# Kernel tuning notes

Hardware: AMD Instinct MI355X
Metric: run time of the kernel (lower is better)

Reference implementation:

```python
import jax, jax.numpy as jnp
import numpy as np

N, E, B_GRAPHS = 50000, 512000, 64
XD, ED, C, H, L = 16, 8, 64, 2, 2
EPS = 1e-5


def setup_inputs() -> dict:
    key = jax.random.key(0)
    ks = jax.random.split(key, 20)
    w = lambda k, shape: jax.random.normal(k, shape, jnp.float32) * 0.1
    return {
        "x": jax.random.normal(ks[0], (N, XD), jnp.float32),
        "edge_attr": jax.random.normal(ks[1], (E, ED), jnp.float32),
        "edge_src": jax.random.randint(ks[2], (E,), 0, N, dtype=jnp.int32),
        "edge_dst": jax.random.randint(ks[3], (E,), 0, N, dtype=jnp.int32),
        "batch": jnp.sort(jax.random.randint(ks[4], (N,), 0, B_GRAPHS, dtype=jnp.int32)),
        "node_W": w(ks[5], (XD, C)), "node_b": jnp.zeros((C,), jnp.float32),
        "edge_W": w(ks[6], (ED, C)), "edge_b": jnp.zeros((C,), jnp.float32),
        "Wq": w(ks[7], (L, C, H * C)), "bq": jnp.zeros((L, H * C), jnp.float32),
        "Wk": w(ks[8], (L, C, H * C)), "bk": jnp.zeros((L, H * C), jnp.float32),
        "Wv": w(ks[9], (L, C, H * C)), "bv": jnp.zeros((L, H * C), jnp.float32),
        "We": w(ks[10], (L, C, H * C)), "be": jnp.zeros((L, H * C), jnp.float32),
        "Wskip": w(ks[11], (L, C, C)), "bskip": jnp.zeros((L, C), jnp.float32),
        "gamma": jnp.ones((L, C), jnp.float32), "beta": jnp.zeros((L, C), jnp.float32),
        "gate_W": w(ks[12], (C, 1)), "gate_b": jnp.zeros((1,), jnp.float32),
        "out_W": w(ks[13], (C, 1)), "out_b": jnp.zeros((1,), jnp.float32),
    }


def reference(x, edge_attr, edge_src, edge_dst, batch,
              node_W, node_b, edge_W, edge_b,
              Wq, bq, Wk, bk, Wv, bv, We, be,
              Wskip, bskip, gamma, beta,
              gate_W, gate_b, out_W, out_b):
    n = x.shape[0]
    h = x @ node_W + node_b                       # node encoder: [N, C]
    e = edge_attr @ edge_W + edge_b               # edge encoder: [E, C]
    scale = 1.0 / jnp.sqrt(jnp.float32(C))
    for i in range(L):
        identity = h
        # TransformerConv (UniMP), concat=False -> mean over heads
        q = (h @ Wq[i] + bq[i]).reshape(n, H, C)
        k = (h @ Wk[i] + bk[i]).reshape(n, H, C)
        v = (h @ Wv[i] + bv[i]).reshape(n, H, C)
        ep = (e @ We[i] + be[i]).reshape(-1, H, C)
        k_e = k[edge_src] + ep                    # [E, H, C]
        v_e = v[edge_src] + ep                    # [E, H, C]
        logits = jnp.einsum('ehc,ehc->eh', q[edge_dst], k_e) * scale
        # segment softmax over incoming edges of each target node
        m = jax.ops.segment_max(logits, edge_dst, num_segments=n)
        a = jnp.exp(logits - m[edge_dst])
        denom = jax.ops.segment_sum(a, edge_dst, num_segments=n)
        alpha = a / denom[edge_dst]               # [E, H]
        agg = jax.ops.segment_sum(alpha[:, :, None] * v_e, edge_dst, num_segments=n)
        out = agg.mean(axis=1) + h @ Wskip[i] + bskip[i]   # root/skip term
        # BatchNorm1d (training mode, biased variance)
        mu = out.mean(axis=0)
        var = out.var(axis=0)
        out = gamma[i] * (out - mu) * jax.lax.rsqrt(var + EPS) + beta[i]
        out = jax.nn.leaky_relu(out, 0.01)
        h = out + identity                        # residual
    # GlobalAttention pooling over graphs
    gate = (h @ gate_W + gate_b)[:, 0]            # [N]
    gm = jax.ops.segment_max(gate, batch, num_segments=B_GRAPHS)
    ge = jnp.exp(gate - gm[batch])
    gd = jax.ops.segment_sum(ge, batch, num_segments=B_GRAPHS)
    wts = ge / gd[batch]
    pooled = jax.ops.segment_sum(wts[:, None] * h, batch, num_segments=B_GRAPHS)
    return jax.nn.sigmoid(pooled @ out_W + out_b)  # [B_GRAPHS, 1]
```

## Files before the change

kernel.cpp:

```cpp
#include <hip/hip_runtime.h>
#include <hip/hip_bf16.h>

typedef unsigned short ushort_t;
typedef __attribute__((ext_vector_type(8))) short short8;
typedef __attribute__((ext_vector_type(4))) float float4v;

__device__ __forceinline__ float bfu_lo(unsigned u) {
    return __uint_as_float(u << 16);
}
__device__ __forceinline__ float bfu_hi(unsigned u) {
    return __uint_as_float(u & 0xffff0000u);
}
__device__ __forceinline__ float bfu_s(ushort_t u) {
    return __uint_as_float(((unsigned)u) << 16);
}
__device__ __forceinline__ ushort_t f2bf(float f) {
    __hip_bfloat16 h = __float2bfloat16(f);
    return *reinterpret_cast<ushort_t*>(&h);
}



__global__ __launch_bounds__(256) void setup_kernel(
    const float* __restrict__ x, const float* __restrict__ node_W,
    const float* __restrict__ node_b,
    const float* __restrict__ edge_W, const float* __restrict__ edge_b,
    const float* __restrict__ We, const float* __restrict__ be,
    const float* __restrict__ Wq, const float* __restrict__ bq,
    const float* __restrict__ Wk, const float* __restrict__ bk,
    const float* __restrict__ Wv, const float* __restrict__ bv,
    const float* __restrict__ Wskip, const float* __restrict__ bskip,
    float* __restrict__ h, ushort_t* __restrict__ h_bf,
    int* __restrict__ counts,
    float* __restrict__ Wc, float* __restrict__ bcb,
    ushort_t* __restrict__ Wall_arr, float* __restrict__ Wall_bias,
    ushort_t* __restrict__ wv_arr,
    int O0, int O1, int O2, int N) {
    int b = blockIdx.x, t = threadIdx.x;
    if (b < O0) {
        int idx = b * 256 + t;
        if (idx < N * 64) {
            int n = idx >> 6, c = idx & 63;
            float acc = node_b[c];
#pragma unroll
            for (int j = 0; j < 16; ++j) acc += x[n * 16 + j] * node_W[j * 64 + c];
            h[idx] = acc;
            h_bf[idx] = f2bf(acc);
        }
    } else if (b < O1) {
        int i = (b - O0) * 256 + t;
        if (i < N) counts[i] = 0;
    } else if (b < O2) {
        int tid = (b - O1) * 256 + t;
        if (tid < 2048) {
            int l = tid >> 10, d = (tid >> 7) & 7, j = tid & 127;
            float s = 0.f;
            for (int m = 0; m < 64; ++m) s += edge_W[d * 64 + m] * We[l * 8192 + m * 128 + j];
            Wc[l * 1024 + d * 128 + j] = s;
        } else if (tid < 2048 + 256) {
            int u = tid - 2048;
            int l = u >> 7, j = u & 127;
            float s = be[l * 128 + j];
            for (int m = 0; m < 64; ++m) s += edge_b[m] * We[l * 8192 + m * 128 + j];
            bcb[l * 128 + j] = s;
        }
    } else {
        int tid = (b - O2) * 256 + t;
        if (tid < 2 * 14336) {
            int l = tid / 14336, u = tid % 14336;
            int j = u & 7, ln = (u >> 3) & 63, kch = (u >> 9) & 1, ct = u >> 10;
            int nn = ln & 15, quad = ln >> 4;
            int k = kch * 32 + quad * 8 + j;
            int col = ct * 16 + nn;
            float v = 0.f;
            if (col < 128) {
                int hh = col >> 6, m = col & 63;
                const float* wq = Wq + l * 8192 + k * 128 + hh * 64;
                const float* wk = Wk + l * 8192 + m * 128 + hh * 64;
                float s = 0.f;
                for (int c2 = 0; c2 < 64; ++c2) s += wq[c2] * wk[c2];
                v = 0.125f * s;
            } else if (col < 192) {
                v = Wskip[l * 4096 + k * 64 + (col - 128)];
            }
            Wall_arr[(size_t)l * 14336 + ct * 1024 + kch * 512 + ln * 8 + j] = f2bf(v);
        } else if (tid < 2 * 14336 + 2 * 224) {
            int u = tid - 2 * 14336;
            int l = u / 224, col = u % 224;
            float v = 0.f;
            if (col < 128) {
                int hh = col >> 6, m = col & 63;
                const float* bqp = bq + l * 128 + hh * 64;
                const float* wk = Wk + l * 8192 + m * 128 + hh * 64;
                float s = 0.f;
                for (int c2 = 0; c2 < 64; ++c2) s += bqp[c2] * wk[c2];
                v = 0.125f * s;
            } else if (col < 192) {
                v = bskip[l * 64 + col - 128];
            }
            Wall_bias[l * 224 + col] = v;
        } else if (tid < 2 * 14336 + 2 * 224 + 2 * 8192) {
            int u = tid - (2 * 14336 + 2 * 224);
            int l = u >> 13, r = u & 8191;
            int j = r & 7, ln = (r >> 3) & 63, ct = (r >> 9) & 3, kc = r >> 11;
            int quad = ln >> 4, nn = ln & 15;
            int p = kc * 32 + quad * 8 + j;
            int hh = p >> 6, m = p & 63;
            int c2 = ct * 16 + nn;
            wv_arr[(size_t)l * 8192 + r] = f2bf(Wv[l * 8192 + m * 128 + hh * 64 + c2]);
        }
    }
}

__global__ void combine2_kernel(const float* __restrict__ Wq, const float* __restrict__ bq,
                                const float* __restrict__ bk, const float* __restrict__ bv,
                                const float* __restrict__ Wc, const float* __restrict__ bcb,
                                ushort_t* __restrict__ Wall_arr, float* __restrict__ Wall_bias,
                                float* __restrict__ cst) {
    int tid = blockIdx.x * 256 + threadIdx.x;
    if (tid < 2304) {
        int l = tid / 1152, u = tid % 1152, k = u / 18, j = u % 18;
        float s = 0.f;
        if (j < 16) {
            int hh = j >> 3, d = j & 7;
            for (int c = 0; c < 64; ++c)
                s += Wq[l * 8192 + k * 128 + hh * 64 + c] * Wc[l * 1024 + d * 128 + hh * 64 + c];
        } else {
            int hh = j - 16;
            for (int c = 0; c < 64; ++c)
                s += Wq[l * 8192 + k * 128 + hh * 64 + c] *
                     (bcb[l * 128 + hh * 64 + c] + bk[l * 128 + hh * 64 + c]);
        }
        s *= 0.125f;
        int col = 192 + j;
        int ct = col >> 4, nn = col & 15;
        int kch = k >> 5, quad = (k >> 3) & 3, jj = k & 7;
        int ln = quad * 16 + nn;
        Wall_arr[(size_t)l * 14336 + ct * 1024 + kch * 512 + ln * 8 + jj] = f2bf(s);
    } else if (tid < 2304 + 36) {
        int u = tid - 2304;
        int l = u / 18, j = u % 18;
        float s = 0.f;
        if (j < 16) {
            int hh = j >> 3, d = j & 7;
            for (int c = 0; c < 64; ++c)
                s += bq[l * 128 + hh * 64 + c] * Wc[l * 1024 + d * 128 + hh * 64 + c];
        } else {
            int hh = j - 16;
            for (int c = 0; c < 64; ++c)
                s += bq[l * 128 + hh * 64 + c] *
                     (bcb[l * 128 + hh * 64 + c] + bk[l * 128 + hh * 64 + c]);
        }
        Wall_bias[l * 224 + 192 + j] = 0.125f * s;
    } else if (tid < 2304 + 36 + 128) {
        int u = tid - 2340;
        int l = u >> 6, c = u & 63;
        cst[l * 64 + c] = 0.5f * (bv[l * 128 + c] + bv[l * 128 + 64 + c] +
                                  bcb[l * 128 + c] + bcb[l * 128 + 64 + c]);
    }
}


__global__ void csr_count_kernel(const int* __restrict__ dst, int* __restrict__ counts, int E) {
    int e = blockIdx.x * 256 + threadIdx.x;
    if (e < E) atomicAdd(&counts[dst[e]], 1);
}

__global__ void scan1_kernel(const int* __restrict__ counts, int* __restrict__ rowptr,
                             int* __restrict__ bsums, int N) {
    __shared__ int s[256];
    int t = threadIdx.x, i = blockIdx.x * 256 + t;
    int v = (i < N) ? counts[i] : 0;
    s[t] = v;
    __syncthreads();
    for (int d = 1; d < 256; d <<= 1) {
        int x = (t >= d) ? s[t - d] : 0;
        __syncthreads();
        s[t] += x;
        __syncthreads();
    }
    if (i < N) rowptr[i] = s[t] - v;
    if (t == 255) bsums[blockIdx.x] = s[255];
}

__global__ void scan3_kernel(int* __restrict__ rowptr, const int* __restrict__ bsums,
                             int* __restrict__ cursor, int N, int E, int nb) {
    __shared__ int sh[256];
    int t = threadIdx.x;
    int v = (t < nb) ? bsums[t] : 0;
    sh[t] = v;
    __syncthreads();
    for (int d = 1; d < 256; d <<= 1) {
        int x = (t >= d) ? sh[t - d] : 0;
        __syncthreads();
        sh[t] += x;
        __syncthreads();
    }
    int blk = blockIdx.x;
    int offv = (blk == 0) ? 0 : sh[blk - 1];
    int i = blk * 256 + t;
    if (i < N) {
        int r = rowptr[i] + offv;
        rowptr[i] = r;
        cursor[i] = r;
    }
    if (i == 0) rowptr[N] = E;
}

__global__ void csr_fill_kernel(const int* __restrict__ dst, const int* __restrict__ src,
                                const float* __restrict__ edge_attr, int* __restrict__ cursor,
                                char* __restrict__ erec, int E) {
    int e = blockIdx.x * 256 + threadIdx.x;
    if (e < E) {
        int pos = atomicAdd(&cursor[dst[e]], 1);
        float4 a0 = *(const float4*)(edge_attr + (size_t)e * 8);
        float4 a1 = *(const float4*)(edge_attr + (size_t)e * 8 + 4);
        uint4 w1;
        w1.x = (unsigned)f2bf(a0.x) | ((unsigned)f2bf(a0.y) << 16);
        w1.y = (unsigned)f2bf(a0.z) | ((unsigned)f2bf(a0.w) << 16);
        w1.z = (unsigned)f2bf(a1.x) | ((unsigned)f2bf(a1.y) << 16);
        w1.w = (unsigned)f2bf(a1.z) | ((unsigned)f2bf(a1.w) << 16);
        char* rp = erec + (size_t)pos * 32;
        *(uint4*)rp = make_uint4((unsigned)(src[e] * 128), 0u, 0u, 0u);
        *(uint4*)(rp + 16) = w1;
    }
}


__global__ __launch_bounds__(512) void layer_kernel(
    const ushort_t* __restrict__ h_bf,
    const char* __restrict__ erec, const int* __restrict__ rowptr,
    const ushort_t* __restrict__ Wall_arr, const float* __restrict__ Wall_bias,
    const ushort_t* __restrict__ wv_arr, const float* __restrict__ Wc,
    const float* __restrict__ cst,
    float* __restrict__ outbuf, float* __restrict__ part, int N) {
    __shared__ ushort_t qk2_s[32][128];
    __shared__ ushort_t ha_s[32][136];
    __shared__ float qc_s[32][20];
    __shared__ float skip_s[32][64];
    __shared__ float sen_s[32][16];
    __shared__ float dw_s[32];
    __shared__ float Wc_s[1024];
    __shared__ float cst_s[64];
    __shared__ float ps[2][128];
    int t = threadIdx.x;
    int lane = t & 63, wid = t >> 6;
    int n0 = blockIdx.x * 32;
    for (int i = t; i < 1024; i += 512) Wc_s[i] = Wc[i];
    if (t < 64) cst_s[t] = cst[t];

    {
        int quad = lane >> 4, nn16 = lane & 15;
        int nodeA = n0 + nn16;      if (nodeA >= N) nodeA = N - 1;
        int nodeB = n0 + 16 + nn16; if (nodeB >= N) nodeB = N - 1;
        const ushort_t* apA = h_bf + (size_t)nodeA * 64 + quad * 8;
        const ushort_t* apB = h_bf + (size_t)nodeB * 64 + quad * 8;
        short8 aA0 = *(const short8*)apA;
        short8 aA1 = *(const short8*)(apA + 32);
        short8 aB0 = *(const short8*)apB;
        short8 aB1 = *(const short8*)(apB + 32);
        for (int ct = wid; ct < 14; ct += 8) {
            const ushort_t* bp = Wall_arr + (size_t)ct * 1024 + lane * 8;
            short8 b0 = *(const short8*)bp;
            short8 b1 = *(const short8*)(bp + 512);
            float4v cA = {0.f, 0.f, 0.f, 0.f};
            float4v cB = {0.f, 0.f, 0.f, 0.f};
            cA = __builtin_amdgcn_mfma_f32_16x16x32_bf16(aA0, b0, cA, 0, 0, 0);
            cA = __builtin_amdgcn_mfma_f32_16x16x32_bf16(aA1, b1, cA, 0, 0, 0);
            cB = __builtin_amdgcn_mfma_f32_16x16x32_bf16(aB0, b0, cB, 0, 0, 0);
            cB = __builtin_amdgcn_mfma_f32_16x16x32_bf16(aB1, b1, cB, 0, 0, 0);
            int col = ct * 16 + nn16;
            float bias = Wall_bias[col];
#pragma unroll
            for (int g = 0; g < 2; ++g) {
                float4v c = g ? cB : cA;
                int lbase = g * 16 + quad * 4;
#pragma unroll
                for (int r = 0; r < 4; ++r) {
                    float v = c[r] + bias;
                    int ln2 = lbase + r;
                    if (col < 128) qk2_s[ln2][col] = f2bf(v);
                    else if (col < 192) skip_s[ln2][col - 128] = v;
                    else if (col < 210) qc_s[ln2][col - 192] = v;
                }
            }
        }
    }
    __syncthreads();

    {
        int grp = lane >> 4, l16 = lane & 15;
        int head = l16 >> 3, l8 = l16 & 7;
        const char* hbb = (const char*)h_bf;
        int ln = wid * 4 + grp;
        int n = n0 + ln;
        bool active = (n < N);
        int nn = active ? n : (N - 1);
        int start = rowptr[nn];
        int deg = active ? (rowptr[nn + 1] - start) : 0;
        int wdeg = deg;
        wdeg = max(wdeg, __shfl_xor(wdeg, 16));
        wdeg = max(wdeg, __shfl_xor(wdeg, 32));

        float lsum = 0.f;
        float se_own = 0.f;
        float hacc[8] = {0.f, 0.f, 0.f, 0.f, 0.f, 0.f, 0.f, 0.f};

        if (wdeg > 0) {
            uint4 qr = *(const uint4*)&qk2_s[ln][head * 64 + l8 * 8];
            float qk0 = bfu_lo(qr.x), qk1 = bfu_hi(qr.x);
            float qk2f = bfu_lo(qr.y), qk3 = bfu_hi(qr.y);
            float qk4 = bfu_lo(qr.z), qk5 = bfu_hi(qr.z);
            float qk6 = bfu_lo(qr.w), qk7 = bfu_hi(qr.w);
            float qcown = qc_s[ln][head * 8 + l8];
            float qb = qc_s[ln][16 + head];

            bool dpos = (deg > 0);
            int dclamp = dpos ? (deg - 1) : 0;
            int base = dpos ? start : 0;

            int offL = *(const int*)(erec + (size_t)(base + min(l16, dclamp)) * 32);
            int o0 = __shfl(offL, grp * 16);
            uint4 ca = *(const uint4*)(hbb + (size_t)(unsigned)o0 + l8 * 16);
            float eaf = bfu_s(*(const ushort_t*)(erec + (size_t)base * 32 + 16 + l8 * 2));

            for (int it = 0; it < wdeg; ++it) {
                int itn = it + 1;
                if ((itn & 15) == 0)
                    offL = *(const int*)(erec + (size_t)(base + min(itn + l16, dclamp)) * 32);
                int itc = min(itn, wdeg - 1);
                int on = __shfl(offL, grp * 16 + (itc & 15));
                uint4 na = *(const uint4*)(hbb + (size_t)(unsigned)on + l8 * 16);
                int gin = base + min(itc, dclamp);
                float fe = bfu_s(*(const ushort_t*)(erec + (size_t)gin * 32 + 16 + l8 * 2));

                float h0 = bfu_lo(ca.x), h1 = bfu_hi(ca.x);
                float h2 = bfu_lo(ca.y), h3 = bfu_hi(ca.y);
                float h4 = bfu_lo(ca.z), h5 = bfu_hi(ca.z);
                float h6 = bfu_lo(ca.w), h7 = bfu_hi(ca.w);
                float dt = qk0 * h0 + qk1 * h1 + qk2f * h2 + qk3 * h3
                         + qk4 * h4 + qk5 * h5 + qk6 * h6 + qk7 * h7
                         + qcown * eaf;
                dt += __shfl_xor(dt, 1);
                dt += __shfl_xor(dt, 2);
                dt += __shfl_xor(dt, 4);
                float s0 = dt + qb;
                float p = (it < deg) ? __expf(fmaxf(s0, -60.f)) : 0.f;
                lsum += p;
                hacc[0] += p * h0; hacc[1] += p * h1;
                hacc[2] += p * h2; hacc[3] += p * h3;
                hacc[4] += p * h4; hacc[5] += p * h5;
                hacc[6] += p * h6; hacc[7] += p * h7;
                se_own += p * eaf;
                ca = na; eaf = fe;
            }
        }

        float inv = (deg > 0) ? (0.5f / lsum) : 0.f;
#pragma unroll
        for (int j2 = 0; j2 < 8; ++j2)
            ha_s[ln][head * 64 + l8 * 8 + j2] = f2bf(hacc[j2] * inv);
        sen_s[ln][head * 8 + l8] = se_own * inv;
        if (l16 == 0) dw_s[ln] = (deg > 0) ? 1.f : 0.f;
    }
    __syncthreads();

    {
        int quad = lane >> 4, nn16 = lane & 15;
        int ct = wid & 3, g = wid >> 2;
        float4v c = {0.f, 0.f, 0.f, 0.f};
#pragma unroll
        for (int kc = 0; kc < 4; ++kc) {
            short8 a = *(const short8*)&ha_s[g * 16 + nn16][kc * 32 + quad * 8];
            short8 b = *(const short8*)(wv_arr + kc * 2048 + ct * 512 + lane * 8);
            c = __builtin_amdgcn_mfma_f32_16x16x32_bf16(a, b, c, 0, 0, 0);
        }
        int col = ct * 16 + nn16;
        float sa = 0.f, sq = 0.f;
#pragma unroll
        for (int r = 0; r < 4; ++r) {
            int ln2 = g * 16 + quad * 4 + r;
            int nr = n0 + ln2;
            const float* sp = sen_s[ln2];
            float ep = 0.f;
#pragma unroll
            for (int hh = 0; hh < 2; ++hh)
#pragma unroll
                for (int d = 0; d < 8; ++d)
                    ep += sp[hh * 8 + d] * Wc_s[d * 128 + hh * 64 + col];
            if (nr < N) {
                float val = c[r] + ep + dw_s[ln2] * cst_s[col] + skip_s[ln2][col];
                outbuf[(size_t)nr * 64 + col] = val;
                sa += val;
                sq += val * val;
            }
        }
        sa += __shfl_xor(sa, 16); sa += __shfl_xor(sa, 32);
        sq += __shfl_xor(sq, 16); sq += __shfl_xor(sq, 32);
        if (quad == 0) { ps[g][col] = sa; ps[g][64 + col] = sq; }
    }
    __syncthreads();
    if (t < 128) part[(size_t)blockIdx.x * 128 + t] = ps[0][t] + ps[1][t];
}


__global__ __launch_bounds__(256) void bnreduce_kernel(const float* __restrict__ part,
                                                       float* __restrict__ bnsums, int nb) {
    int s = blockIdx.x;
    int t = threadIdx.x;
    float a = 0.f;
    for (int b = t; b < nb; b += 256) a += part[(size_t)b * 128 + s];
    __shared__ float sh[256];
    sh[t] = a;
    __syncthreads();
    for (int d = 128; d; d >>= 1) {
        if (t < d) sh[t] += sh[t + d];
        __syncthreads();
    }
    if (t == 0) bnsums[s] = sh[0];
}

__global__ __launch_bounds__(256) void bnh_kernel(
    const float* __restrict__ outbuf, const float* __restrict__ bnsums,
    const float* __restrict__ gamma, const float* __restrict__ beta,
    float* __restrict__ h, ushort_t* __restrict__ h_bf, int N) {
    int idx = blockIdx.x * 256 + threadIdx.x;
    if (idx >= N * 64) return;
    int c = idx & 63;
    float invN = 1.f / (float)N;
    float mean = bnsums[c] * invN;
    float var = bnsums[64 + c] * invN - mean * mean;
    float scale = gamma[c] * rsqrtf(var + 1e-5f);
    float shift = beta[c] - mean * scale;
    float o = outbuf[idx] * scale + shift;
    o = (o > 0.f) ? o : 0.01f * o;
    float hn = h[idx] + o;
    h[idx] = hn;
    h_bf[idx] = f2bf(hn);
}

__global__ __launch_bounds__(256) void bnapply_kernel(
    const float* __restrict__ outbuf, const float* __restrict__ bnsums,
    const float* __restrict__ gamma, const float* __restrict__ beta,
    const float* __restrict__ gate_W, const float* __restrict__ gate_b,
    float* __restrict__ h, float* __restrict__ gatebuf, int N) {
    int idx = blockIdx.x * 256 + threadIdx.x;
    if (idx >= N * 64) return;
    int c = idx & 63, n = idx >> 6;
    float invN = 1.f / (float)N;
    float mean = bnsums[c] * invN;
    float var = bnsums[64 + c] * invN - mean * mean;
    float scale = gamma[c] * rsqrtf(var + 1e-5f);
    float shift = beta[c] - mean * scale;
    float o = outbuf[idx] * scale + shift;
    o = (o > 0.f) ? o : 0.01f * o;
    float hn = h[idx] + o;
    h[idx] = hn;
    float g = hn * gate_W[c];
#pragma unroll
    for (int off = 32; off; off >>= 1) g += __shfl_xor(g, off);
    if (c == 0) gatebuf[n] = g + gate_b[0];
}


__global__ __launch_bounds__(256) void pool_acc_kernel(
    const float* __restrict__ h, const float* __restrict__ gatebuf,
    const int* __restrict__ batch,
    float* __restrict__ pacc, float* __restrict__ pden, int N) {
    int b = blockIdx.x >> 3, chunk = blockIdx.x & 7;
    int lo = 0, hi = N;
    while (lo < hi) { int mid = (lo + hi) >> 1; if (batch[mid] < b) lo = mid + 1; else hi = mid; }
    int start = lo;
    lo = start; hi = N;
    while (lo < hi) { int mid = (lo + hi) >> 1; if (batch[mid] <= b) lo = mid + 1; else hi = mid; }
    int end = lo;
    int t = threadIdx.x, lane = t & 63, wid = t >> 6;
    __shared__ float sm[4];
    float mx = -1e30f;
    for (int n = start + t; n < end; n += 256) mx = fmaxf(mx, gatebuf[n]);
#pragma unroll
    for (int off = 32; off; off >>= 1) mx = fmaxf(mx, __shfl_xor(mx, off));
    if (lane == 0) sm[wid] = mx;
    __syncthreads();
    float mb = fmaxf(fmaxf(sm[0], sm[1]), fmaxf(sm[2], sm[3]));
    int gwid = chunk * 4 + wid;
    float acc = 0.f, den = 0.f;
    for (int n = start + gwid; n < end; n += 32) {
        float ge = __expf(gatebuf[n] - mb);
        acc += ge * h[(size_t)n * 64 + lane];
        den += ge;
    }
    __shared__ float sacc[4][64];
    __shared__ float sden[4];
    sacc[wid][lane] = acc;
    if (lane == 0) sden[wid] = den;
    __syncthreads();
    if (wid == 0) {
        pacc[(size_t)blockIdx.x * 64 + lane] =
            sacc[0][lane] + sacc[1][lane] + sacc[2][lane] + sacc[3][lane];
        if (lane == 0) pden[blockIdx.x] = sden[0] + sden[1] + sden[2] + sden[3];
    }
}

__global__ void pool_fin_kernel(const float* __restrict__ pacc, const float* __restrict__ pden,
                                const float* __restrict__ out_W, const float* __restrict__ out_b,
                                float* __restrict__ out) {
    int b = blockIdx.x, c = threadIdx.x;
    float pc = 0.f, dv = 0.f;
#pragma unroll
    for (int j = 0; j < 8; ++j) {
        pc += pacc[(size_t)(b * 8 + j) * 64 + c];
        dv += pden[b * 8 + j];
    }
    float s = pc * out_W[c];
#pragma unroll
    for (int off = 32; off; off >>= 1) s += __shfl_xor(s, off);
    if (c == 0) {
        if (dv <= 0.f) dv = 1.f;
        float v = s / dv + out_b[0];
        out[b] = 1.f / (1.f + __expf(-v));
    }
}


extern "C" void kernel_launch(void* const* d_in, const int* in_sizes, int n_in,
                              void* d_out, int out_size, void* d_ws, size_t ws_size,
                              hipStream_t stream) {
    const float* x         = (const float*)d_in[0];
    const float* edge_attr = (const float*)d_in[1];
    const int*   edge_src  = (const int*)d_in[2];
    const int*   edge_dst  = (const int*)d_in[3];
    const int*   batch     = (const int*)d_in[4];
    const float* node_W    = (const float*)d_in[5];
    const float* node_b    = (const float*)d_in[6];
    const float* edge_W    = (const float*)d_in[7];
    const float* edge_b    = (const float*)d_in[8];
    const float* Wq        = (const float*)d_in[9];
    const float* bq        = (const float*)d_in[10];
    const float* Wk        = (const float*)d_in[11];
    const float* bk        = (const float*)d_in[12];
    const float* Wv        = (const float*)d_in[13];
    const float* bv        = (const float*)d_in[14];
    const float* We        = (const float*)d_in[15];
    const float* be        = (const float*)d_in[16];
    const float* Wskip     = (const float*)d_in[17];
    const float* bskip     = (const float*)d_in[18];
    const float* gamma     = (const float*)d_in[19];
    const float* beta      = (const float*)d_in[20];
    const float* gate_W    = (const float*)d_in[21];
    const float* gate_b    = (const float*)d_in[22];
    const float* out_W     = (const float*)d_in[23];
    const float* out_b     = (const float*)d_in[24];
    float* out = (float*)d_out;

    const int N = in_sizes[0] / 16;
    const int E = in_sizes[2];
    const int nbl = (N + 31) / 32;

    char* ws = (char*)d_ws;
    size_t off = 0;
    auto alloc = [&](size_t bytes) {
        size_t o = off;
        off += (bytes + 255) & ~(size_t)255;
        return o;
    };
    float*    h        = (float*)(ws + alloc((size_t)N * 64 * 4));
    ushort_t* h_bf     = (ushort_t*)(ws + alloc((size_t)N * 64 * 2));
    float*    outbuf   = (float*)(ws + alloc((size_t)N * 64 * 4));
    int*      rowptr   = (int*)(ws + alloc((size_t)(N + 1) * 4));
    int*      cursor   = (int*)(ws + alloc((size_t)N * 4));
    int*      counts   = (int*)(ws + alloc((size_t)N * 4));
    int*      bsums    = (int*)(ws + alloc(1024));
    char*     erec     = (char*)(ws + alloc((size_t)E * 32));
    float*    Wc       = (float*)(ws + alloc(2 * 1024 * 4));
    float*    bcb      = (float*)(ws + alloc(2 * 128 * 4));
    ushort_t* Wall_arr = (ushort_t*)(ws + alloc(2 * 14336 * 2));
    float*    Wall_b   = (float*)(ws + alloc(2 * 224 * 4));
    ushort_t* wv_arr   = (ushort_t*)(ws + alloc(2 * 8192 * 2));
    float*    cst      = (float*)(ws + alloc(2 * 64 * 4));
    float*    bnsums   = (float*)(ws + alloc(128 * 4));
    float*    gatebuf  = (float*)(ws + alloc((size_t)N * 4));
    float*    part     = (float*)(ws + alloc((size_t)nbl * 128 * 4));
    float*    pacc     = (float*)(ws + alloc((size_t)512 * 64 * 4));
    float*    pden     = (float*)(ws + alloc(512 * 4));
    if (off > ws_size) return;

    int O0 = (N * 64 + 255) / 256;
    int O1 = O0 + (N + 255) / 256;
    int O2 = O1 + 9;
    int O3 = O2 + 178;
    setup_kernel<<<O3, 256, 0, stream>>>(
        x, node_W, node_b, edge_W, edge_b, We, be, Wq, bq, Wk, bk, Wv, bv, Wskip, bskip,
        h, h_bf, counts, Wc, bcb, Wall_arr, Wall_b, wv_arr, O0, O1, O2, N);
    combine2_kernel<<<10, 256, 0, stream>>>(Wq, bq, bk, bv, Wc, bcb, Wall_arr, Wall_b, cst);

    csr_count_kernel<<<(E + 255) / 256, 256, 0, stream>>>(edge_dst, counts, E);
    int nb = (N + 255) / 256;
    scan1_kernel<<<nb, 256, 0, stream>>>(counts, rowptr, bsums, N);
    scan3_kernel<<<nb, 256, 0, stream>>>(rowptr, bsums, cursor, N, E, nb);
    csr_fill_kernel<<<(E + 255) / 256, 256, 0, stream>>>(edge_dst, edge_src, edge_attr,
                                                         cursor, erec, E);

    layer_kernel<<<nbl, 512, 0, stream>>>(h_bf, erec, rowptr,
                                          Wall_arr, Wall_b, wv_arr, Wc, cst,
                                          outbuf, part, N);
    bnreduce_kernel<<<128, 256, 0, stream>>>(part, bnsums, nbl);
    bnh_kernel<<<(N * 64 + 255) / 256, 256, 0, stream>>>(
        outbuf, bnsums, gamma, beta, h, h_bf, N);

    layer_kernel<<<nbl, 512, 0, stream>>>(h_bf, erec, rowptr,
                                          Wall_arr + 14336, Wall_b + 224, wv_arr + 8192,
                                          Wc + 1024, cst + 64,
                                          outbuf, part, N);
    bnreduce_kernel<<<128, 256, 0, stream>>>(part, bnsums, nbl);
    bnapply_kernel<<<(N * 64 + 255) / 256, 256, 0, stream>>>(
        outbuf, bnsums, gamma + 64, beta + 64, gate_W, gate_b, h, gatebuf, N);

    pool_acc_kernel<<<512, 256, 0, stream>>>(h, gatebuf, batch, pacc, pden, N);
    pool_fin_kernel<<<64, 64, 0, stream>>>(pacc, pden, out_W, out_b, out);
}
```

Measured before the change: 329.4 us.

## Sort nodes by degree within block and deepen gather prefetch to two

```diff
diff --git a/kernel.cpp b/kernel.cpp
--- a/kernel.cpp
+++ b/kernel.cpp
@@ -243,6 +243,7 @@
     __shared__ float Wc_s[1024];
     __shared__ float cst_s[64];
     __shared__ float ps[2][128];
+    __shared__ int perm_s[32];
     int t = threadIdx.x;
     int lane = t & 63, wid = t >> 6;
     int n0 = blockIdx.x * 32;
@@ -288,11 +289,24 @@
     }
     __syncthreads();
 
+    if (t < 32) {
+        int nc = n0 + t;
+        int d = (nc < N) ? (rowptr[nc + 1] - rowptr[nc]) : 0;
+        int r = 0;
+#pragma unroll
+        for (int m = 0; m < 32; ++m) {
+            int dm = __shfl(d, m);
+            r += (dm > d || (dm == d && m < t)) ? 1 : 0;
+        }
+        perm_s[r] = t;
+    }
+    __syncthreads();
+
     {
         int grp = lane >> 4, l16 = lane & 15;
         int head = l16 >> 3, l8 = l16 & 7;
         const char* hbb = (const char*)h_bf;
-        int ln = wid * 4 + grp;
+        int ln = perm_s[wid * 4 + grp];
         int n = n0 + ln;
         bool active = (n < N);
         int nn = active ? n : (N - 1);
@@ -321,26 +335,31 @@
 
             int offL = *(const int*)(erec + (size_t)(base + min(l16, dclamp)) * 32);
             int o0 = __shfl(offL, grp * 16);
-            uint4 ca = *(const uint4*)(hbb + (size_t)(unsigned)o0 + l8 * 16);
-            float eaf = bfu_s(*(const ushort_t*)(erec + (size_t)base * 32 + 16 + l8 * 2));
+            uint4 ca0 = *(const uint4*)(hbb + (size_t)(unsigned)o0 + l8 * 16);
+            float ea0 = bfu_s(*(const ushort_t*)(erec + (size_t)base * 32 + 16 + l8 * 2));
+            int q1 = min(1, wdeg - 1);
+            int o1 = __shfl(offL, grp * 16 + q1);
+            uint4 ca1 = *(const uint4*)(hbb + (size_t)(unsigned)o1 + l8 * 16);
+            int g1 = base + min(q1, dclamp);
+            float ea1 = bfu_s(*(const ushort_t*)(erec + (size_t)g1 * 32 + 16 + l8 * 2));
 
             for (int it = 0; it < wdeg; ++it) {
-                int itn = it + 1;
-                if ((itn & 15) == 0)
-                    offL = *(const int*)(erec + (size_t)(base + min(itn + l16, dclamp)) * 32);
-                int itc = min(itn, wdeg - 1);
-                int on = __shfl(offL, grp * 16 + (itc & 15));
-                uint4 na = *(const uint4*)(hbb + (size_t)(unsigned)on + l8 * 16);
-                int gin = base + min(itc, dclamp);
-                float fe = bfu_s(*(const ushort_t*)(erec + (size_t)gin * 32 + 16 + l8 * 2));
-
-                float h0 = bfu_lo(ca.x), h1 = bfu_hi(ca.x);
-                float h2 = bfu_lo(ca.y), h3 = bfu_hi(ca.y);
-                float h4 = bfu_lo(ca.z), h5 = bfu_hi(ca.z);
-                float h6 = bfu_lo(ca.w), h7 = bfu_hi(ca.w);
+                int p2 = it + 2;
+                if ((p2 & 15) == 0 && p2 < wdeg)
+                    offL = *(const int*)(erec + (size_t)(base + min(p2 + l16, dclamp)) * 32);
+                int q2 = min(p2, wdeg - 1);
+                int on = __shfl(offL, grp * 16 + (q2 & 15));
+                uint4 ca2 = *(const uint4*)(hbb + (size_t)(unsigned)on + l8 * 16);
+                int g2 = base + min(q2, dclamp);
+                float ea2 = bfu_s(*(const ushort_t*)(erec + (size_t)g2 * 32 + 16 + l8 * 2));
+
+                float h0 = bfu_lo(ca0.x), h1 = bfu_hi(ca0.x);
+                float h2 = bfu_lo(ca0.y), h3 = bfu_hi(ca0.y);
+                float h4 = bfu_lo(ca0.z), h5 = bfu_hi(ca0.z);
+                float h6 = bfu_lo(ca0.w), h7 = bfu_hi(ca0.w);
                 float dt = qk0 * h0 + qk1 * h1 + qk2f * h2 + qk3 * h3
                          + qk4 * h4 + qk5 * h5 + qk6 * h6 + qk7 * h7
-                         + qcown * eaf;
+                         + qcown * ea0;
                 dt += __shfl_xor(dt, 1);
                 dt += __shfl_xor(dt, 2);
                 dt += __shfl_xor(dt, 4);
@@ -351,8 +370,9 @@
                 hacc[2] += p * h2; hacc[3] += p * h3;
                 hacc[4] += p * h4; hacc[5] += p * h5;
                 hacc[6] += p * h6; hacc[7] += p * h7;
-                se_own += p * eaf;
-                ca = na; eaf = fe;
+                se_own += p * ea0;
+                ca0 = ca1; ea0 = ea1;
+                ca1 = ca2; ea1 = ea2;
             }
         }
 
```

New measurement: 325.0 us. Within noise of the previous version (-1.4%).
